# Optimization experiments

Measured on AMD Instinct MI355X. Metric: run time of the kernel, lower is better.

## Reference

```python
import jax, jax.numpy as jnp
import numpy as np

N, T, H = 4000, 32, 64      # N = batch_size*n_neurons, t_repetition, gcn_d
E = 1024000
NT = N * T                   # graph nodes after temporal unrolling
N_NEURONS = 500
B = N // N_NEURONS
T_EBD = 16                   # tau * t_repetition = 0.5*32
N_STEPS = 12


def setup_inputs() -> dict:
    key = jax.random.key(0)
    ks = jax.random.split(key, 13)
    s = 1.0 / np.sqrt(H)
    return {
        "node_features": jax.random.normal(ks[0], (N, T, H), jnp.float32),
        "edge_index_batch": jax.random.randint(ks[1], (2, E), 0, NT, jnp.int32),
        "edge_attr_batch": jax.random.uniform(ks[2], (E,), jnp.float32),
        "batch": jax.random.randint(ks[3], (N,), 0, B, jnp.int32),
        # GRU params (1 layer, torch layout: W_ih [3H,H], W_hh [3H,H])
        "gru_Wih": jax.random.normal(ks[4], (3 * H, H), jnp.float32) * s,
        "gru_Whh": jax.random.normal(ks[5], (3 * H, H), jnp.float32) * s,
        "gru_bih": jax.random.normal(ks[6], (3 * H,), jnp.float32) * s,
        "gru_bhh": jax.random.normal(ks[7], (3 * H,), jnp.float32) * s,
        # GCNConv linear weight [out,in], no bias
        "gcn_W": jax.random.normal(ks[8], (H, H), jnp.float32) * s,
        # temporal attention MLP: Linear(T->T_ebd), Linear(T_ebd->T), no bias
        "attn_W1": jax.random.normal(ks[9], (T_EBD, T), jnp.float32) * (1.0 / np.sqrt(T)),
        "attn_W2": jax.random.normal(ks[10], (T, T_EBD), jnp.float32) * (1.0 / np.sqrt(T_EBD)),
        # final head Linear(gcn_d -> n_steps) with bias
        "fc_W": jax.random.normal(ks[11], (N_STEPS, H), jnp.float32) * s,
        "fc_b": jax.random.normal(ks[12], (N_STEPS,), jnp.float32) * s,
    }


def _gru(x, Wih, Whh, bih, bhh):
    # x: [N, T, H] -> outputs [N, T, H] (torch GRU equations, h0 = 0)
    xg = x @ Wih.T + bih  # [N, T, 3H], input projection precomputed

    def step(h, xg_t):
        hg = h @ Whh.T + bhh
        xr, xz, xn = jnp.split(xg_t, 3, axis=-1)
        hr, hz, hn = jnp.split(hg, 3, axis=-1)
        r = jax.nn.sigmoid(xr + hr)
        z = jax.nn.sigmoid(xz + hz)
        n = jnp.tanh(xn + r * hn)
        h_new = (1.0 - z) * n + z * h
        return h_new, h_new

    h0 = jnp.zeros((x.shape[0], Whh.shape[1]), x.dtype)
    _, hs = jax.lax.scan(step, h0, jnp.swapaxes(xg, 0, 1))  # hs: [T, N, H]
    return jnp.swapaxes(hs, 0, 1)


def _gcn(x, W, edge_index, edge_weight, n_nodes):
    # PyG GCNConv: add self-loops (weight 1), symmetric deg^-1/2 norm, no bias
    loops = jnp.arange(n_nodes, dtype=edge_index.dtype)
    src = jnp.concatenate([edge_index[0], loops])
    dst = jnp.concatenate([edge_index[1], loops])
    w = jnp.concatenate([edge_weight, jnp.ones((n_nodes,), edge_weight.dtype)])
    xw = x @ W.T                                            # [NT, H]
    deg = jax.ops.segment_sum(w, dst, num_segments=n_nodes)
    dis = jnp.where(deg > 0, jax.lax.rsqrt(jnp.where(deg > 0, deg, 1.0)), 0.0)
    norm = dis[src] * w * dis[dst]                          # [E+NT]
    msgs = norm[:, None] * xw[src]                          # gather + scale
    return jax.ops.segment_sum(msgs, dst, num_segments=n_nodes)


def reference(node_features, edge_index_batch, edge_attr_batch, batch,
              gru_Wih, gru_Whh, gru_bih, gru_bhh, gcn_W,
              attn_W1, attn_W2, fc_W, fc_b):
    # DGRLayer: GRU over time, then GCN over the flattened (node,time) graph
    g = _gru(node_features, gru_Wih, gru_Whh, gru_bih, gru_bhh)  # [N, T, H]
    x = g.reshape(NT, H)
    x = _gcn(x, gcn_W, edge_index_batch, edge_attr_batch, NT)
    x3 = x.reshape(N, T, H)

    # TemporalAttention (reshape mirrors torch contiguous .view semantics)
    xt = x3.reshape(B, T, N_NEURONS * H).mean(axis=-1)           # [B, T]
    attn = jax.nn.sigmoid(jax.nn.relu(xt @ attn_W1.T) @ attn_W2.T)  # [B, T]

    nf = x3.reshape(B, T, N_NEURONS, H)
    pooled = jnp.sum(attn[:, :, None, None] * nf, axis=(1, 2))   # [B, H]
    return pooled @ fc_W.T + fc_b                                # [B, n_steps]
```

## Files before the change

### kernel.cpp

```cpp
#include <hip/hip_runtime.h>
#include <hip/hip_fp16.h>

#define NNODES   4000
#define TSTEPS   32
#define HDIM     64
#define ECOUNT   1024000
#define NTOT     128000
#define BATCHB   8
#define NNEUR    500
#define TEBD     16
#define NSTEPS   12

#define CNT_SHIFT 44
#define SUM_MASK  ((1ull << CNT_SHIFT) - 1ull)
#define SLOTS     32
#define REC_BLOCKS (NNODES / 16)

typedef _Float16 half8_t __attribute__((ext_vector_type(8)));
typedef float    f32x4_t __attribute__((ext_vector_type(4)));

__device__ __forceinline__ float sigmoidf_(float x) {
    return 1.0f / (1.0f + __expf(-x));
}
__device__ __forceinline__ float tanhf_(float x) {
    return 1.0f - 2.0f / (1.0f + __expf(2.0f * x));
}

__global__ __launch_bounds__(256) void k_recHist(
    const float* __restrict__ x, const float* __restrict__ Wih,
    const float* __restrict__ Whh, const float* __restrict__ bih,
    const float* __restrict__ bhh, const float* __restrict__ Wg,
    _Float16* __restrict__ xwh,
    const int* __restrict__ ei, const float* __restrict__ ea,
    unsigned long long* __restrict__ dc, int2* __restrict__ se32)
{
    __shared__ __align__(16) _Float16 hbuf[2][16 * 72];

    const int tid = threadIdx.x;

    if (blockIdx.x >= REC_BLOCKS) {
        int e = (blockIdx.x - REC_BLOCKS) * 256 + tid;
        int s = ei[e], d = ei[ECOUNT + e];
        float w = ea[e];
        unsigned long long fx = (unsigned long long)(w * 4294967296.0f + 0.5f);
        unsigned long long old = atomicAdd(&dc[d], (1ull << CNT_SHIFT) | fx);
        int r = (int)(old >> CNT_SHIFT);
        if (r < SLOTS)
            se32[d * SLOTS + r] = make_int2(s, __float_as_int(w));
        return;
    }

    const int lane = tid & 63;
    const int wv   = tid >> 6;
    const int c    = lane & 15;
    const int quad = lane >> 4;
    const int n0   = blockIdx.x * 16;

    auto makeB = [&](const float* W, int row, int k0) -> half8_t {
        const float4* p = (const float4*)(W + (size_t)row * HDIM + k0);
        float4 u = p[0], v = p[1];
        half8_t h;
        h[0] = (_Float16)u.x; h[1] = (_Float16)u.y; h[2] = (_Float16)u.z; h[3] = (_Float16)u.w;
        h[4] = (_Float16)v.x; h[5] = (_Float16)v.y; h[6] = (_Float16)v.z; h[7] = (_Float16)v.w;
        return h;
    };

    half8_t Bxr[2], Bxz[2], Bxn[2], Bhr[2], Bhz[2], Bhn[2], Bw[2];
#pragma unroll
    for (int kt = 0; kt < 2; ++kt) {
        int k0 = kt * 32 + quad * 8;
        Bxr[kt] = makeB(Wih, wv * 16 + c, k0);
        Bxz[kt] = makeB(Wih, 64 + wv * 16 + c, k0);
        Bxn[kt] = makeB(Wih, 128 + wv * 16 + c, k0);
        Bhr[kt] = makeB(Whh, wv * 16 + c, k0);
        Bhz[kt] = makeB(Whh, 64 + wv * 16 + c, k0);
        Bhn[kt] = makeB(Whh, 128 + wv * 16 + c, k0);
        Bw[kt]  = makeB(Wg, wv * 16 + c, k0);
    }

    const int f = wv * 16 + c;
    const float brz_r = bih[f] + bhh[f];
    const float brz_z = bih[64 + f] + bhh[64 + f];
    const float bin_  = bih[128 + f];
    const float bhn_  = bhh[128 + f];

    float hreg[4] = {0.f, 0.f, 0.f, 0.f};
    half8_t ah[2];

    const float* xp = x + (size_t)(n0 + c) * (TSTEPS * HDIM) + quad * 8;

    float4 xq0[4], xq1[4];
    {
        const float* p0 = xp;
        xq0[0] = *(const float4*)(p0);      xq0[1] = *(const float4*)(p0 + 4);
        xq0[2] = *(const float4*)(p0 + 32); xq0[3] = *(const float4*)(p0 + 36);
        const float* p1 = xp + HDIM;
        xq1[0] = *(const float4*)(p1);      xq1[1] = *(const float4*)(p1 + 4);
        xq1[2] = *(const float4*)(p1 + 32); xq1[3] = *(const float4*)(p1 + 36);
    }

    auto step = [&](int t, float4* xq) {
        half8_t ax[2];
#pragma unroll
        for (int kt = 0; kt < 2; ++kt) {
            float4 u = xq[kt * 2], v = xq[kt * 2 + 1];
            half8_t a;
            a[0] = (_Float16)u.x; a[1] = (_Float16)u.y; a[2] = (_Float16)u.z; a[3] = (_Float16)u.w;
            a[4] = (_Float16)v.x; a[5] = (_Float16)v.y; a[6] = (_Float16)v.z; a[7] = (_Float16)v.w;
            ax[kt] = a;
        }
        if (t + 2 < TSTEPS) {
            const float* pt = xp + (size_t)(t + 2) * HDIM;
            xq[0] = *(const float4*)(pt);      xq[1] = *(const float4*)(pt + 4);
            xq[2] = *(const float4*)(pt + 32); xq[3] = *(const float4*)(pt + 36);
        }

        f32x4_t Cr  = (f32x4_t){0.f, 0.f, 0.f, 0.f};
        f32x4_t Cz  = (f32x4_t){0.f, 0.f, 0.f, 0.f};
        f32x4_t Cnx = (f32x4_t){0.f, 0.f, 0.f, 0.f};
        f32x4_t Cnh = (f32x4_t){0.f, 0.f, 0.f, 0.f};

#pragma unroll
        for (int kt = 0; kt < 2; ++kt) {
            Cr  = __builtin_amdgcn_mfma_f32_16x16x32_f16(ax[kt], Bxr[kt], Cr, 0, 0, 0);
            Cz  = __builtin_amdgcn_mfma_f32_16x16x32_f16(ax[kt], Bxz[kt], Cz, 0, 0, 0);
            Cnx = __builtin_amdgcn_mfma_f32_16x16x32_f16(ax[kt], Bxn[kt], Cnx, 0, 0, 0);
        }
        if (t > 0) {
#pragma unroll
            for (int kt = 0; kt < 2; ++kt) {
                Cr  = __builtin_amdgcn_mfma_f32_16x16x32_f16(ah[kt], Bhr[kt], Cr, 0, 0, 0);
                Cz  = __builtin_amdgcn_mfma_f32_16x16x32_f16(ah[kt], Bhz[kt], Cz, 0, 0, 0);
                Cnh = __builtin_amdgcn_mfma_f32_16x16x32_f16(ah[kt], Bhn[kt], Cnh, 0, 0, 0);
            }
        }

        _Float16* hb = hbuf[t & 1];
#pragma unroll
        for (int r = 0; r < 4; ++r) {
            float rr = sigmoidf_(Cr[r] + brz_r);
            float zz = sigmoidf_(Cz[r] + brz_z);
            float nn = tanhf_(Cnx[r] + bin_ + rr * (Cnh[r] + bhn_));
            float hn = (1.0f - zz) * nn + zz * hreg[r];
            hreg[r] = hn;
            hb[(quad * 4 + r) * 72 + f] = (_Float16)hn;
        }

        __syncthreads();

#pragma unroll
        for (int kt = 0; kt < 2; ++kt)
            ah[kt] = *(half8_t*)&hb[c * 72 + kt * 32 + quad * 8];

        f32x4_t Cw = (f32x4_t){0.f, 0.f, 0.f, 0.f};
#pragma unroll
        for (int kt = 0; kt < 2; ++kt)
            Cw = __builtin_amdgcn_mfma_f32_16x16x32_f16(ah[kt], Bw[kt], Cw, 0, 0, 0);

#pragma unroll
        for (int r = 0; r < 4; ++r) {
            int row = (n0 + quad * 4 + r) * TSTEPS + t;
            xwh[(size_t)row * HDIM + f] = (_Float16)Cw[r];
        }
    };

#pragma unroll 1
    for (int tt = 0; tt < TSTEPS; tt += 2) {
        step(tt, xq0);
        step(tt + 1, xq1);
    }
}

__global__ void k_dis(const unsigned long long* __restrict__ dc,
                      float* __restrict__ dis) {
    int i = blockIdx.x * blockDim.x + threadIdx.x;
    if (i < NTOT) {
        float deg = 1.0f + (float)(dc[i] & SUM_MASK) * 0x1p-32f;
        dis[i] = rsqrtf(deg);
    }
}

__global__ __launch_bounds__(256) void k_gather(
    const _Float16* __restrict__ xwh, const unsigned long long* __restrict__ dc,
    const int2* __restrict__ se32, const float* __restrict__ dis,
    _Float16* __restrict__ y)
{
    const int lane = threadIdx.x & 63;
    const int d = blockIdx.x * 4 + (threadIdx.x >> 6);
    const float dd = dis[d];
    int cnt = (int)(dc[d] >> CNT_SHIFT);
    cnt = cnt < SLOTS ? cnt : SLOTS;
    const int2* bkt = se32 + (size_t)d * SLOTS;

    float a0 = dd * (float)xwh[(size_t)d * HDIM + lane];
    float a1 = 0.f, a2 = 0.f, a3 = 0.f;
    int j = 0;
    for (; j + 4 <= cnt; j += 4) {
        int2 e0 = bkt[j], e1 = bkt[j + 1], e2 = bkt[j + 2], e3 = bkt[j + 3];
        float c0 = dis[e0.x] * __int_as_float(e0.y);
        float c1 = dis[e1.x] * __int_as_float(e1.y);
        float c2 = dis[e2.x] * __int_as_float(e2.y);
        float c3 = dis[e3.x] * __int_as_float(e3.y);
        float v0 = (float)xwh[(size_t)e0.x * HDIM + lane];
        float v1 = (float)xwh[(size_t)e1.x * HDIM + lane];
        float v2 = (float)xwh[(size_t)e2.x * HDIM + lane];
        float v3 = (float)xwh[(size_t)e3.x * HDIM + lane];
        a0 = fmaf(c0, v0, a0);
        a1 = fmaf(c1, v1, a1);
        a2 = fmaf(c2, v2, a2);
        a3 = fmaf(c3, v3, a3);
    }
    for (; j < cnt; ++j) {
        int2 e = bkt[j];
        a0 = fmaf(dis[e.x] * __int_as_float(e.y),
                  (float)xwh[(size_t)e.x * HDIM + lane], a0);
    }
    y[(size_t)d * HDIM + lane] = (_Float16)(dd * ((a0 + a1) + (a2 + a3)));
}

__global__ __launch_bounds__(256) void k_S(const _Float16* __restrict__ y,
                                           float* __restrict__ S) {
    const int bt = blockIdx.x;
    const int tid = threadIdx.x;
    const int h = tid & 63, g = tid >> 6;
    const _Float16* base = y + (size_t)bt * (NNEUR * HDIM);
    float acc = 0.f;
    for (int n = g; n < NNEUR; n += 4) acc += (float)base[n * HDIM + h];
    __shared__ float red[256];
    red[tid] = acc;
    __syncthreads();
    if (tid < 64)
        S[bt * 64 + tid] = red[tid] + red[64 + tid] + red[128 + tid] + red[192 + tid];
}

__global__ __launch_bounds__(256) void k_final(
    const float* __restrict__ S, const float* __restrict__ W1,
    const float* __restrict__ W2, const float* __restrict__ fcW,
    const float* __restrict__ fcb, float* __restrict__ out)
{
    __shared__ float xt[256];
    __shared__ float a1[128];
    __shared__ float attn[256];
    __shared__ float pooled[512];
    const int tid = threadIdx.x;

    {
        float s = 0.f;
        const float* p = S + tid * 64;
#pragma unroll
        for (int hh = 0; hh < 64; ++hh) s += p[hh];
        xt[tid] = s * (1.0f / 32000.0f);
    }
    __syncthreads();
    if (tid < 128) {
        int b = tid >> 4, i = tid & 15;
        float s = 0.f;
#pragma unroll
        for (int t = 0; t < 32; ++t) s += xt[b * 32 + t] * W1[i * 32 + t];
        a1[tid] = fmaxf(s, 0.f);
    }
    __syncthreads();
    {
        int b = tid >> 5, t = tid & 31;
        float s = 0.f;
#pragma unroll
        for (int i = 0; i < 16; ++i) s += a1[b * 16 + i] * W2[t * 16 + i];
        attn[tid] = 1.0f / (1.0f + __expf(-s));
    }
    __syncthreads();
    for (int o = tid; o < 512; o += 256) {
        int b = o >> 6, h = o & 63;
        float s = 0.f;
#pragma unroll
        for (int t = 0; t < 32; ++t) s += attn[b * 32 + t] * S[(b * 32 + t) * 64 + h];
        pooled[o] = s;
    }
    __syncthreads();
    if (tid < BATCHB * NSTEPS) {
        int b = tid / NSTEPS, st = tid % NSTEPS;
        float acc = fcb[st];
#pragma unroll
        for (int h = 0; h < 64; ++h) acc += pooled[b * 64 + h] * fcW[st * 64 + h];
        out[b * NSTEPS + st] = acc;
    }
}

extern "C" void kernel_launch(void* const* d_in, const int* in_sizes, int n_in,
                              void* d_out, int out_size, void* d_ws, size_t ws_size,
                              hipStream_t stream) {
    const float* x   = (const float*)d_in[0];
    const int*   ei  = (const int*)  d_in[1];
    const float* ea  = (const float*)d_in[2];
    const float* Wih = (const float*)d_in[4];
    const float* Whh = (const float*)d_in[5];
    const float* bih = (const float*)d_in[6];
    const float* bhh = (const float*)d_in[7];
    const float* Wg  = (const float*)d_in[8];
    const float* W1  = (const float*)d_in[9];
    const float* W2  = (const float*)d_in[10];
    const float* fcW = (const float*)d_in[11];
    const float* fcb = (const float*)d_in[12];
    float* out = (float*)d_out;

    char* p = (char*)d_ws;
    unsigned long long* dc = (unsigned long long*)p; p += sizeof(unsigned long long) * NTOT;
    int2*  se32 = (int2*)p;        p += sizeof(int2) * (size_t)NTOT * SLOTS;
    _Float16* xwh = (_Float16*)p;  p += sizeof(_Float16) * (size_t)NTOT * HDIM;
    _Float16* y   = (_Float16*)p;  p += sizeof(_Float16) * (size_t)NTOT * HDIM;
    float* dis = (float*)p;        p += sizeof(float) * NTOT;
    float* S   = (float*)p;

    hipMemsetAsync(dc, 0, sizeof(unsigned long long) * NTOT, stream);
    k_recHist <<<REC_BLOCKS + ECOUNT / 256, 256, 0, stream>>>(
        x, Wih, Whh, bih, bhh, Wg, xwh, ei, ea, dc, se32);
    k_dis     <<<(NTOT + 255) / 256, 256, 0, stream>>>(dc, dis);
    k_gather  <<<NTOT / 4, 256, 0, stream>>>(xwh, dc, se32, dis, y);
    k_S       <<<256, 256, 0, stream>>>(y, S);
    k_final   <<<1, 256, 0, stream>>>(S, W1, W2, fcW, fcb, out);
}
```

Before: 273.8 us.

## Fuse degree normalization into gather, widen recurrent blocks to 512 threads

Removes the separate k_dis kernel and computes rsqrt of each node's degree inside the gather, reading the packed count/sum word directly for both the destination and each source. The gather loop is restructured into 8-wide predicated batches with eight independent accumulators to raise memory-level parallelism. The GRU/histogram kernel now uses 512-thread blocks holding two 16-node groups, which halves the block count and shares weight loading per block. In exchange, the gather recomputes rsqrt per edge and issues padded loads for inactive slots, and the larger blocks could change occupancy.

```diff
diff --git a/kernel.cpp b/kernel.cpp
--- a/kernel.cpp
+++ b/kernel.cpp
@@ -14,7 +14,8 @@
 #define CNT_SHIFT 44
 #define SUM_MASK  ((1ull << CNT_SHIFT) - 1ull)
 #define SLOTS     32
-#define REC_BLOCKS (NNODES / 16)
+#define REC_BLOCKS (NNODES / 32)
+#define HIST_BLOCKS (ECOUNT / 512)
 
 typedef _Float16 half8_t __attribute__((ext_vector_type(8)));
 typedef float    f32x4_t __attribute__((ext_vector_type(4)));
@@ -26,7 +27,7 @@
     return 1.0f - 2.0f / (1.0f + __expf(2.0f * x));
 }
 
-__global__ __launch_bounds__(256) void k_recHist(
+__global__ __launch_bounds__(512) void k_recHist(
     const float* __restrict__ x, const float* __restrict__ Wih,
     const float* __restrict__ Whh, const float* __restrict__ bih,
     const float* __restrict__ bhh, const float* __restrict__ Wg,
@@ -34,12 +35,12 @@
     const int* __restrict__ ei, const float* __restrict__ ea,
     unsigned long long* __restrict__ dc, int2* __restrict__ se32)
 {
-    __shared__ __align__(16) _Float16 hbuf[2][16 * 72];
+    __shared__ __align__(16) _Float16 hbuf[2][32 * 72];
 
     const int tid = threadIdx.x;
 
     if (blockIdx.x >= REC_BLOCKS) {
-        int e = (blockIdx.x - REC_BLOCKS) * 256 + tid;
+        int e = (blockIdx.x - REC_BLOCKS) * 512 + tid;
         int s = ei[e], d = ei[ECOUNT + e];
         float w = ea[e];
         unsigned long long fx = (unsigned long long)(w * 4294967296.0f + 0.5f);
@@ -52,9 +53,11 @@
 
     const int lane = tid & 63;
     const int wv   = tid >> 6;
+    const int grp  = wv >> 2;
+    const int st   = wv & 3;
     const int c    = lane & 15;
     const int quad = lane >> 4;
-    const int n0   = blockIdx.x * 16;
+    const int n0   = blockIdx.x * 32 + grp * 16;
 
     auto makeB = [&](const float* W, int row, int k0) -> half8_t {
         const float4* p = (const float4*)(W + (size_t)row * HDIM + k0);
@@ -69,16 +72,16 @@
 #pragma unroll
     for (int kt = 0; kt < 2; ++kt) {
         int k0 = kt * 32 + quad * 8;
-        Bxr[kt] = makeB(Wih, wv * 16 + c, k0);
-        Bxz[kt] = makeB(Wih, 64 + wv * 16 + c, k0);
-        Bxn[kt] = makeB(Wih, 128 + wv * 16 + c, k0);
-        Bhr[kt] = makeB(Whh, wv * 16 + c, k0);
-        Bhz[kt] = makeB(Whh, 64 + wv * 16 + c, k0);
-        Bhn[kt] = makeB(Whh, 128 + wv * 16 + c, k0);
-        Bw[kt]  = makeB(Wg, wv * 16 + c, k0);
-    }
-
-    const int f = wv * 16 + c;
+        Bxr[kt] = makeB(Wih, st * 16 + c, k0);
+        Bxz[kt] = makeB(Wih, 64 + st * 16 + c, k0);
+        Bxn[kt] = makeB(Wih, 128 + st * 16 + c, k0);
+        Bhr[kt] = makeB(Whh, st * 16 + c, k0);
+        Bhz[kt] = makeB(Whh, 64 + st * 16 + c, k0);
+        Bhn[kt] = makeB(Whh, 128 + st * 16 + c, k0);
+        Bw[kt]  = makeB(Wg, st * 16 + c, k0);
+    }
+
+    const int f = st * 16 + c;
     const float brz_r = bih[f] + bhh[f];
     const float brz_z = bih[64 + f] + bhh[64 + f];
     const float bin_  = bih[128 + f];
@@ -88,6 +91,8 @@
     half8_t ah[2];
 
     const float* xp = x + (size_t)(n0 + c) * (TSTEPS * HDIM) + quad * 8;
+    _Float16* hb0 = &hbuf[0][grp * 16 * 72];
+    _Float16* hb1 = &hbuf[1][grp * 16 * 72];
 
     float4 xq0[4], xq1[4];
     {
@@ -99,7 +104,7 @@
         xq1[2] = *(const float4*)(p1 + 32); xq1[3] = *(const float4*)(p1 + 36);
     }
 
-    auto step = [&](int t, float4* xq) {
+    auto step = [&](int t, float4* xq, _Float16* hb) {
         half8_t ax[2];
 #pragma unroll
         for (int kt = 0; kt < 2; ++kt) {
@@ -135,7 +140,6 @@
             }
         }
 
-        _Float16* hb = hbuf[t & 1];
 #pragma unroll
         for (int r = 0; r < 4; ++r) {
             float rr = sigmoidf_(Cr[r] + brz_r);
@@ -166,56 +170,46 @@
 
 #pragma unroll 1
     for (int tt = 0; tt < TSTEPS; tt += 2) {
-        step(tt, xq0);
-        step(tt + 1, xq1);
-    }
-}
-
-__global__ void k_dis(const unsigned long long* __restrict__ dc,
-                      float* __restrict__ dis) {
-    int i = blockIdx.x * blockDim.x + threadIdx.x;
-    if (i < NTOT) {
-        float deg = 1.0f + (float)(dc[i] & SUM_MASK) * 0x1p-32f;
-        dis[i] = rsqrtf(deg);
+        step(tt, xq0, hb0);
+        step(tt + 1, xq1, hb1);
     }
 }
 
 __global__ __launch_bounds__(256) void k_gather(
     const _Float16* __restrict__ xwh, const unsigned long long* __restrict__ dc,
-    const int2* __restrict__ se32, const float* __restrict__ dis,
-    _Float16* __restrict__ y)
+    const int2* __restrict__ se32, _Float16* __restrict__ y)
 {
     const int lane = threadIdx.x & 63;
     const int d = blockIdx.x * 4 + (threadIdx.x >> 6);
-    const float dd = dis[d];
-    int cnt = (int)(dc[d] >> CNT_SHIFT);
+    const unsigned long long dcd = dc[d];
+    int cnt = (int)(dcd >> CNT_SHIFT);
     cnt = cnt < SLOTS ? cnt : SLOTS;
+    const float dd = rsqrtf(1.0f + (float)(dcd & SUM_MASK) * 0x1p-32f);
     const int2* bkt = se32 + (size_t)d * SLOTS;
 
-    float a0 = dd * (float)xwh[(size_t)d * HDIM + lane];
-    float a1 = 0.f, a2 = 0.f, a3 = 0.f;
-    int j = 0;
-    for (; j + 4 <= cnt; j += 4) {
-        int2 e0 = bkt[j], e1 = bkt[j + 1], e2 = bkt[j + 2], e3 = bkt[j + 3];
-        float c0 = dis[e0.x] * __int_as_float(e0.y);
-        float c1 = dis[e1.x] * __int_as_float(e1.y);
-        float c2 = dis[e2.x] * __int_as_float(e2.y);
-        float c3 = dis[e3.x] * __int_as_float(e3.y);
-        float v0 = (float)xwh[(size_t)e0.x * HDIM + lane];
-        float v1 = (float)xwh[(size_t)e1.x * HDIM + lane];
-        float v2 = (float)xwh[(size_t)e2.x * HDIM + lane];
-        float v3 = (float)xwh[(size_t)e3.x * HDIM + lane];
-        a0 = fmaf(c0, v0, a0);
-        a1 = fmaf(c1, v1, a1);
-        a2 = fmaf(c2, v2, a2);
-        a3 = fmaf(c3, v3, a3);
-    }
-    for (; j < cnt; ++j) {
-        int2 e = bkt[j];
-        a0 = fmaf(dis[e.x] * __int_as_float(e.y),
-                  (float)xwh[(size_t)e.x * HDIM + lane], a0);
-    }
-    y[(size_t)d * HDIM + lane] = (_Float16)(dd * ((a0 + a1) + (a2 + a3)));
+    float acc[8];
+    acc[0] = dd * (float)xwh[(size_t)d * HDIM + lane];
+#pragma unroll
+    for (int k = 1; k < 8; ++k) acc[k] = 0.f;
+
+#pragma unroll 1
+    for (int j = 0; j < cnt; j += 8) {
+#pragma unroll
+        for (int k = 0; k < 8; ++k) {
+            int jj = j + k;
+            int2 e = bkt[jj < SLOTS ? jj : SLOTS - 1];
+            bool val = jj < cnt;
+            int src = val ? e.x : d;
+            float w = val ? __int_as_float(e.y) : 0.f;
+            unsigned long long dcs = dc[src];
+            float ds = rsqrtf(1.0f + (float)(dcs & SUM_MASK) * 0x1p-32f);
+            float v = (float)xwh[(size_t)src * HDIM + lane];
+            acc[k] = fmaf(ds * w, v, acc[k]);
+        }
+    }
+    float s = ((acc[0] + acc[1]) + (acc[2] + acc[3]))
+            + ((acc[4] + acc[5]) + (acc[6] + acc[7]));
+    y[(size_t)d * HDIM + lane] = (_Float16)(dd * s);
 }
 
 __global__ __launch_bounds__(256) void k_S(const _Float16* __restrict__ y,
@@ -307,14 +301,12 @@
     int2*  se32 = (int2*)p;        p += sizeof(int2) * (size_t)NTOT * SLOTS;
     _Float16* xwh = (_Float16*)p;  p += sizeof(_Float16) * (size_t)NTOT * HDIM;
     _Float16* y   = (_Float16*)p;  p += sizeof(_Float16) * (size_t)NTOT * HDIM;
-    float* dis = (float*)p;        p += sizeof(float) * NTOT;
     float* S   = (float*)p;
 
     hipMemsetAsync(dc, 0, sizeof(unsigned long long) * NTOT, stream);
-    k_recHist <<<REC_BLOCKS + ECOUNT / 256, 256, 0, stream>>>(
+    k_recHist <<<REC_BLOCKS + HIST_BLOCKS, 512, 0, stream>>>(
         x, Wih, Whh, bih, bhh, Wg, xwh, ei, ea, dc, se32);
-    k_dis     <<<(NTOT + 255) / 256, 256, 0, stream>>>(dc, dis);
-    k_gather  <<<NTOT / 4, 256, 0, stream>>>(xwh, dc, se32, dis, y);
+    k_gather  <<<NTOT / 4, 256, 0, stream>>>(xwh, dc, se32, y);
     k_S       <<<256, 256, 0, stream>>>(y, S);
     k_final   <<<1, 256, 0, stream>>>(S, W1, W2, fcW, fcb, out);
 }
```

Result: slower. 320.8 us (+17.1%).

## Pre-convert inputs to fp16, fuse degree zeroing, and predicate gather unrolled by eight

Applied to the files above, without the earlier changes.

Adds a prep kernel that converts node features to fp16 and zeroes the degree counters, replacing the memset. The recurrent kernel then loads half-precision inputs, which halves the bytes it reads on its serial path. The gather loop is rewritten as a predicated eight-wide unroll with eight accumulators to keep more loads in flight, and the fp16 buffer is reused as the output y. The cost is an extra full pass over x, and padded lanes make redundant loads of the destination row.

```diff
diff --git a/kernel.cpp b/kernel.cpp
--- a/kernel.cpp
+++ b/kernel.cpp
@@ -6,6 +6,7 @@
 #define HDIM     64
 #define ECOUNT   1024000
 #define NTOT     128000
+#define XELEMS   (NNODES * TSTEPS * HDIM)
 #define BATCHB   8
 #define NNEUR    500
 #define TEBD     16
@@ -15,6 +16,7 @@
 #define SUM_MASK  ((1ull << CNT_SHIFT) - 1ull)
 #define SLOTS     32
 #define REC_BLOCKS (NNODES / 16)
+#define HIST_BLOCKS (ECOUNT / 256)
 
 typedef _Float16 half8_t __attribute__((ext_vector_type(8)));
 typedef float    f32x4_t __attribute__((ext_vector_type(4)));
@@ -26,8 +28,24 @@
     return 1.0f - 2.0f / (1.0f + __expf(2.0f * x));
 }
 
+__global__ __launch_bounds__(256) void k_prep(const float* __restrict__ x,
+                                              _Float16* __restrict__ xh,
+                                              unsigned long long* __restrict__ dc) {
+    int g = blockIdx.x * blockDim.x + threadIdx.x;
+    if (g < NTOT) dc[g] = 0ull;
+    int i = g * 8;
+    if (i < XELEMS) {
+        const float4* p = (const float4*)(x + i);
+        float4 u = p[0], v = p[1];
+        half8_t h;
+        h[0] = (_Float16)u.x; h[1] = (_Float16)u.y; h[2] = (_Float16)u.z; h[3] = (_Float16)u.w;
+        h[4] = (_Float16)v.x; h[5] = (_Float16)v.y; h[6] = (_Float16)v.z; h[7] = (_Float16)v.w;
+        *(half8_t*)(xh + i) = h;
+    }
+}
+
 __global__ __launch_bounds__(256) void k_recHist(
-    const float* __restrict__ x, const float* __restrict__ Wih,
+    const _Float16* __restrict__ xh, const float* __restrict__ Wih,
     const float* __restrict__ Whh, const float* __restrict__ bih,
     const float* __restrict__ bhh, const float* __restrict__ Wg,
     _Float16* __restrict__ xwh,
@@ -87,32 +105,24 @@
     float hreg[4] = {0.f, 0.f, 0.f, 0.f};
     half8_t ah[2];
 
-    const float* xp = x + (size_t)(n0 + c) * (TSTEPS * HDIM) + quad * 8;
-
-    float4 xq0[4], xq1[4];
-    {
-        const float* p0 = xp;
-        xq0[0] = *(const float4*)(p0);      xq0[1] = *(const float4*)(p0 + 4);
-        xq0[2] = *(const float4*)(p0 + 32); xq0[3] = *(const float4*)(p0 + 36);
-        const float* p1 = xp + HDIM;
-        xq1[0] = *(const float4*)(p1);      xq1[1] = *(const float4*)(p1 + 4);
-        xq1[2] = *(const float4*)(p1 + 32); xq1[3] = *(const float4*)(p1 + 36);
-    }
-
-    auto step = [&](int t, float4* xq) {
+    const _Float16* xp = xh + (size_t)(n0 + c) * (TSTEPS * HDIM) + quad * 8;
+
+    half8_t xq0[2], xq1[2];
+#pragma unroll
+    for (int kt = 0; kt < 2; ++kt) {
+        xq0[kt] = *(const half8_t*)(xp + kt * 32);
+        xq1[kt] = *(const half8_t*)(xp + HDIM + kt * 32);
+    }
+
+    auto step = [&](int t, half8_t* xq) {
         half8_t ax[2];
 #pragma unroll
-        for (int kt = 0; kt < 2; ++kt) {
-            float4 u = xq[kt * 2], v = xq[kt * 2 + 1];
-            half8_t a;
-            a[0] = (_Float16)u.x; a[1] = (_Float16)u.y; a[2] = (_Float16)u.z; a[3] = (_Float16)u.w;
-            a[4] = (_Float16)v.x; a[5] = (_Float16)v.y; a[6] = (_Float16)v.z; a[7] = (_Float16)v.w;
-            ax[kt] = a;
-        }
+        for (int kt = 0; kt < 2; ++kt) ax[kt] = xq[kt];
         if (t + 2 < TSTEPS) {
-            const float* pt = xp + (size_t)(t + 2) * HDIM;
-            xq[0] = *(const float4*)(pt);      xq[1] = *(const float4*)(pt + 4);
-            xq[2] = *(const float4*)(pt + 32); xq[3] = *(const float4*)(pt + 36);
+            const _Float16* pt = xp + (size_t)(t + 2) * HDIM;
+#pragma unroll
+            for (int kt = 0; kt < 2; ++kt)
+                xq[kt] = *(const half8_t*)(pt + kt * 32);
         }
 
         f32x4_t Cr  = (f32x4_t){0.f, 0.f, 0.f, 0.f};
@@ -192,30 +202,28 @@
     cnt = cnt < SLOTS ? cnt : SLOTS;
     const int2* bkt = se32 + (size_t)d * SLOTS;
 
-    float a0 = dd * (float)xwh[(size_t)d * HDIM + lane];
-    float a1 = 0.f, a2 = 0.f, a3 = 0.f;
-    int j = 0;
-    for (; j + 4 <= cnt; j += 4) {
-        int2 e0 = bkt[j], e1 = bkt[j + 1], e2 = bkt[j + 2], e3 = bkt[j + 3];
-        float c0 = dis[e0.x] * __int_as_float(e0.y);
-        float c1 = dis[e1.x] * __int_as_float(e1.y);
-        float c2 = dis[e2.x] * __int_as_float(e2.y);
-        float c3 = dis[e3.x] * __int_as_float(e3.y);
-        float v0 = (float)xwh[(size_t)e0.x * HDIM + lane];
-        float v1 = (float)xwh[(size_t)e1.x * HDIM + lane];
-        float v2 = (float)xwh[(size_t)e2.x * HDIM + lane];
-        float v3 = (float)xwh[(size_t)e3.x * HDIM + lane];
-        a0 = fmaf(c0, v0, a0);
-        a1 = fmaf(c1, v1, a1);
-        a2 = fmaf(c2, v2, a2);
-        a3 = fmaf(c3, v3, a3);
-    }
-    for (; j < cnt; ++j) {
-        int2 e = bkt[j];
-        a0 = fmaf(dis[e.x] * __int_as_float(e.y),
-                  (float)xwh[(size_t)e.x * HDIM + lane], a0);
-    }
-    y[(size_t)d * HDIM + lane] = (_Float16)(dd * ((a0 + a1) + (a2 + a3)));
+    float acc[8];
+    acc[0] = dd * (float)xwh[(size_t)d * HDIM + lane];
+#pragma unroll
+    for (int k = 1; k < 8; ++k) acc[k] = 0.f;
+
+#pragma unroll 1
+    for (int j = 0; j < cnt; j += 8) {
+#pragma unroll
+        for (int k = 0; k < 8; ++k) {
+            int jj = j + k;
+            int2 e = bkt[jj < SLOTS ? jj : SLOTS - 1];
+            bool val = jj < cnt;
+            int src = val ? e.x : d;
+            float w = val ? __int_as_float(e.y) : 0.f;
+            float cf = dis[src] * w;
+            float v = (float)xwh[(size_t)src * HDIM + lane];
+            acc[k] = fmaf(cf, v, acc[k]);
+        }
+    }
+    float s = ((acc[0] + acc[1]) + (acc[2] + acc[3]))
+            + ((acc[4] + acc[5]) + (acc[6] + acc[7]));
+    y[(size_t)d * HDIM + lane] = (_Float16)(dd * s);
 }
 
 __global__ __launch_bounds__(256) void k_S(const _Float16* __restrict__ y,
@@ -305,14 +313,15 @@
     char* p = (char*)d_ws;
     unsigned long long* dc = (unsigned long long*)p; p += sizeof(unsigned long long) * NTOT;
     int2*  se32 = (int2*)p;        p += sizeof(int2) * (size_t)NTOT * SLOTS;
+    _Float16* xh  = (_Float16*)p;  p += sizeof(_Float16) * (size_t)XELEMS;
     _Float16* xwh = (_Float16*)p;  p += sizeof(_Float16) * (size_t)NTOT * HDIM;
-    _Float16* y   = (_Float16*)p;  p += sizeof(_Float16) * (size_t)NTOT * HDIM;
     float* dis = (float*)p;        p += sizeof(float) * NTOT;
     float* S   = (float*)p;
-
-    hipMemsetAsync(dc, 0, sizeof(unsigned long long) * NTOT, stream);
-    k_recHist <<<REC_BLOCKS + ECOUNT / 256, 256, 0, stream>>>(
-        x, Wih, Whh, bih, bhh, Wg, xwh, ei, ea, dc, se32);
+    _Float16* y = xh;
+
+    k_prep    <<<(XELEMS / 8 + 255) / 256, 256, 0, stream>>>(x, xh, dc);
+    k_recHist <<<REC_BLOCKS + HIST_BLOCKS, 256, 0, stream>>>(
+        xh, Wih, Whh, bih, bhh, Wg, xwh, ei, ea, dc, se32);
     k_dis     <<<(NTOT + 255) / 256, 256, 0, stream>>>(dc, dis);
     k_gather  <<<NTOT / 4, 256, 0, stream>>>(xwh, dc, se32, dis, y);
     k_S       <<<256, 256, 0, stream>>>(y, S);
```

Result: slower. 301.2 us (+10.0%).
